# Optimization experiments

Measured on AMD Instinct MI355X. Metric: run time of the kernel, lower is better.

The kernel has to match this reference:

```python
import jax, jax.numpy as jnp
import numpy as np

B, C, H, W = 8, 256, 128, 128
SH, SW = 8, 8            # stoken_size
HH, WW = H // SH, W // SW
NH = 8                   # num_heads
HD = C // NH             # head_dim = 32
KD = HD                  # key_dim (attn_ratio=1)
ATTN_SCALE = KD ** (-0.5)
AFF_SCALE = C ** (-0.5)


def unfold9(x):
    """x: (B,C,hh,ww) -> (B, hh*ww, C, 9); matches Unfold(3) + transpose/reshape."""
    b, c, hh, ww = x.shape
    xp = jnp.pad(x, ((0, 0), (0, 0), (1, 1), (1, 1)))
    p = jnp.stack([xp[:, :, dy:dy + hh, dx:dx + ww]
                   for dy in range(3) for dx in range(3)], axis=2)  # (B,C,9,hh,ww)
    return p.transpose(0, 3, 4, 1, 2).reshape(b, hh * ww, c, 9)


def fold9(y):
    """y: (B,C,9,hh,ww) -> (B,C,hh,ww); matches Fold(3) (conv_transpose with identity kernels)."""
    hh, ww = y.shape[-2:]
    yp = jnp.pad(y, ((0, 0), (0, 0), (0, 0), (1, 1), (1, 1)))
    out = 0.
    for dy in range(3):
        for dx in range(3):
            out = out + yp[:, :, dy * 3 + dx, 2 - dy:2 - dy + hh, 2 - dx:2 - dx + ww]
    return out


def attention(sf, w_qkv, w_pe, w_proj):
    """Attention module with attn_ratio=1 (Conv layers have act=False, BN identity)."""
    b, c, hh, ww = sf.shape
    n = hh * ww
    qkv = jnp.einsum('oc,bchw->bohw', w_qkv, sf).reshape(b, NH, 2 * KD + HD, n)
    q, k, v = jnp.split(qkv, [KD, 2 * KD], axis=2)
    attn = jax.nn.softmax(jnp.einsum('bhkn,bhkm->bhnm', q, k) * ATTN_SCALE, axis=-1)
    o = jnp.einsum('bhdm,bhnm->bhdn', v, attn).reshape(b, c, hh, ww)
    pe = jax.lax.conv_general_dilated(
        v.reshape(b, c, hh, ww), w_pe, (1, 1), ((1, 1), (1, 1)),
        dimension_numbers=('NCHW', 'OIHW', 'NCHW'), feature_group_count=c)
    return jnp.einsum('oc,bchw->bohw', w_proj, o + pe)


def setup_inputs() -> dict:
    key = jax.random.key(0)
    k0, k1, k2, k3 = jax.random.split(key, 4)
    x = jax.random.normal(k0, (B, C, H, W), dtype=jnp.float32)
    w_qkv = jax.random.normal(k1, (3 * C, C), dtype=jnp.float32) * 0.05
    w_pe = jax.random.normal(k2, (C, 1, 3, 3), dtype=jnp.float32) * 0.05
    w_proj = jax.random.normal(k3, (C, C), dtype=jnp.float32) * 0.05
    return {'x': x, 'w_qkv': w_qkv, 'w_pe': w_pe, 'w_proj': w_proj}


def reference(x, w_qkv, w_pe, w_proj):
    # H,W divisible by stoken_size -> no padding branch
    xb = x.reshape(B, C, HH, SH, WW, SW)
    stoken = xb.mean(axis=(3, 5))                                   # (B,C,hh,ww) adaptive_avg_pool2d
    pix = xb.transpose(0, 2, 4, 3, 5, 1).reshape(B, HH * WW, SH * SW, C)
    # --- single no-grad iteration (n_iter=1) ---
    sf9 = unfold9(stoken)                                            # (B,n,C,9)
    aff = jax.nn.softmax(jnp.einsum('bnpc,bnck->bnpk', pix, sf9) * AFF_SCALE, axis=-1)
    aff = jax.lax.stop_gradient(aff)                                 # torch.no_grad
    asum = aff.sum(axis=2).transpose(0, 2, 1).reshape(B, 1, 9, HH, WW)
    asum = jax.lax.stop_gradient(fold9(asum))                        # (B,1,hh,ww)
    # --- super-token aggregation ---
    sf = jnp.einsum('bnpc,bnpk->bnck', pix, aff)                     # (B,n,C,9)
    sf = fold9(sf.transpose(0, 2, 3, 1).reshape(B, C, 9, HH, WW))    # (B,C,hh,ww)
    sf = sf / (asum + 1e-12)
    # --- refine with attention ---
    sf = attention(sf, w_qkv, w_pe, w_proj)
    # --- scatter back to pixels ---
    sf9b = unfold9(sf)                                               # (B,n,C,9)
    pix_out = jnp.einsum('bnck,bnpk->bnpc', sf9b, aff)               # (B,n,h*w,C)
    return pix_out.reshape(B, HH, WW, C, SH, SW).transpose(0, 3, 1, 4, 2, 5).reshape(B, C, H, W)
```

## Files before the change

### kernel.cpp

```cpp
#include <hip/hip_runtime.h>
#include <cstdint>
#include <cstddef>


#define AFF_SCALE 0.0625f
#define ATTN_SCALE 0.17677669529663687f

__global__ __launch_bounds__(128) void stoken_kernel(
    const float* __restrict__ x, float* __restrict__ stok_pad)
{
    int blk = blockIdx.x;
    int i  = blk & 15;
    int bc = blk >> 4;
    int t  = threadIdx.x;
    const float* xr = x + ((size_t)bc * 128 + i * 8) * 128 + t;
    float s = 0.f;
#pragma unroll
    for (int r = 0; r < 8; ++r) s += xr[r * 128];
    s += __shfl_down(s, 4, 64);
    s += __shfl_down(s, 2, 64);
    s += __shfl_down(s, 1, 64);
    if ((t & 7) == 0) {
        int j = t >> 3;
        int b = bc >> 8, c = bc & 255;
        stok_pad[(((size_t)b * 18 + (i + 1)) * 18 + (j + 1)) * 256 + c] =
            s * (1.f / 64.f);
    }
}

__global__ __launch_bounds__(256) void aff_agg_kernel(
    const float* __restrict__ x, const float* __restrict__ stok_pad,
    float* __restrict__ aff_g, float* __restrict__ asum_g,
    float* __restrict__ agg)
{
    __shared__ __align__(16) float pixs[256 * 68];
    __shared__ __align__(16) float sfs[9 * 260];
    __shared__ __align__(16) float part[576];

    int bid  = blockIdx.x;
    int xcd  = bid & 7, slot_ = bid >> 3;
    int pair = xcd * 128 + (slot_ >> 1);
    int m = pair & 7, i = (pair >> 3) & 15, b = pair >> 7;
    int j = m * 2 + (slot_ & 1);
    int bn = b * 256 + i * 16 + j;
    int t = threadIdx.x;

    {
        int c0 = t >> 3, pi = t & 7;
#pragma unroll
        for (int it = 0; it < 8; ++it) {
            int c = c0 + 32 * it;
            const float* xp = x + (((size_t)b * 256 + c) * 128 + i * 8 + pi) * 128 + j * 8;
            float4 f0 = *(const float4*)&xp[0];
            float4 f1 = *(const float4*)&xp[4];
            int gma = (c >> 2) & 3;
            int s0 = (2 * pi) ^ gma, s1 = (2 * pi + 1) ^ gma;
            *(float4*)&pixs[c * 68 + s0 * 4] = f0;
            *(float4*)&pixs[c * 68 + s1 * 4] = f1;
        }
    }
    {
        const float* spT = stok_pad + (size_t)b * 324 * 256;
#pragma unroll
        for (int dy = 0; dy < 3; ++dy)
#pragma unroll
            for (int dx = 0; dx < 3; ++dx)
                sfs[(dy * 3 + dx) * 260 + t] =
                    spT[((size_t)(i + dy) * 18 + (j + dx)) * 256 + t];
    }
    part[t] = 0.f;
    part[t + 256] = 0.f;
    if (t < 64) part[t + 512] = 0.f;
    __syncthreads();

    int w = t >> 6, l = t & 63;

    {
        int pq = l >> 2, cgl = l & 3;
        int cbase = w * 64 + cgl * 16;
        float acc[4][9];
#pragma unroll
        for (int ii = 0; ii < 4; ++ii)
#pragma unroll
            for (int k = 0; k < 9; ++k) acc[ii][k] = 0.f;

#pragma unroll
        for (int c4i = 0; c4i < 4; ++c4i) {
            int c = cbase + c4i * 4;
            int slot = (pq ^ c4i) * 4;
            const float4 p0 = *(const float4*)&pixs[(c + 0) * 68 + slot];
            const float4 p1 = *(const float4*)&pixs[(c + 1) * 68 + slot];
            const float4 p2 = *(const float4*)&pixs[(c + 2) * 68 + slot];
            const float4 p3 = *(const float4*)&pixs[(c + 3) * 68 + slot];
#pragma unroll
            for (int k = 0; k < 9; ++k) {
                const float4 sv = *(const float4*)&sfs[k * 260 + c];
                acc[0][k] += p0.x * sv.x + p1.x * sv.y + p2.x * sv.z + p3.x * sv.w;
                acc[1][k] += p0.y * sv.x + p1.y * sv.y + p2.y * sv.z + p3.y * sv.w;
                acc[2][k] += p0.z * sv.x + p1.z * sv.y + p2.z * sv.z + p3.z * sv.w;
                acc[3][k] += p0.w * sv.x + p1.w * sv.y + p2.w * sv.z + p3.w * sv.w;
            }
        }
#pragma unroll
        for (int ii = 0; ii < 4; ++ii)
#pragma unroll
            for (int k = 0; k < 9; ++k) {
                acc[ii][k] += __shfl_xor(acc[ii][k], 1, 64);
                acc[ii][k] += __shfl_xor(acc[ii][k], 2, 64);
            }
#pragma unroll
        for (int k = 0; k < 9; ++k) {
            float v01 = (cgl & 1) ? acc[1][k] : acc[0][k];
            float v23 = (cgl & 1) ? acc[3][k] : acc[2][k];
            float vk  = (cgl & 2) ? v23 : v01;
            atomicAdd(&part[l * 9 + k], vk);
        }
    }
    __syncthreads();

    float* affs = sfs;

    if (t < 64) {
        float a[9];
        float mx = -1e30f;
#pragma unroll
        for (int k = 0; k < 9; ++k) {
            float v = part[t * 9 + k] * AFF_SCALE;
            a[k] = v;
            mx = fmaxf(mx, v);
        }
        float ssum = 0.f;
#pragma unroll
        for (int k = 0; k < 9; ++k) { a[k] = __expf(a[k] - mx); ssum += a[k]; }
        float inv = 1.f / ssum;
#pragma unroll
        for (int k = 0; k < 9; ++k) {
            a[k] *= inv;
            affs[k * 64 + t] = a[k];
            aff_g[(size_t)bn * 576 + k * 64 + t] = a[k];
        }
#pragma unroll
        for (int k = 0; k < 9; ++k) {
            float r = a[k];
            r += __shfl_down(r, 32, 64); r += __shfl_down(r, 16, 64);
            r += __shfl_down(r, 8, 64);  r += __shfl_down(r, 4, 64);
            r += __shfl_down(r, 2, 64);  r += __shfl_down(r, 1, 64);
            if (t == 0) asum_g[(size_t)bn * 9 + k] = r;
        }
    }
    __syncthreads();

    {
        int cql = l >> 2, pq2 = l & 3;
        int cb2 = w * 64 + cql * 4;
        int gma = cql & 3;
        float acc2[4][9];
#pragma unroll
        for (int ii = 0; ii < 4; ++ii)
#pragma unroll
            for (int k = 0; k < 9; ++k) acc2[ii][k] = 0.f;

#pragma unroll
        for (int pp = 0; pp < 4; ++pp) {
            int p4 = pq2 * 4 + pp;
            int slot = (p4 ^ gma) * 4;
            const float4 q0 = *(const float4*)&pixs[(cb2 + 0) * 68 + slot];
            const float4 q1 = *(const float4*)&pixs[(cb2 + 1) * 68 + slot];
            const float4 q2 = *(const float4*)&pixs[(cb2 + 2) * 68 + slot];
            const float4 q3 = *(const float4*)&pixs[(cb2 + 3) * 68 + slot];
#pragma unroll
            for (int k = 0; k < 9; ++k) {
                const float4 av = *(const float4*)&affs[k * 64 + p4 * 4];
                acc2[0][k] += q0.x * av.x + q0.y * av.y + q0.z * av.z + q0.w * av.w;
                acc2[1][k] += q1.x * av.x + q1.y * av.y + q1.z * av.z + q1.w * av.w;
                acc2[2][k] += q2.x * av.x + q2.y * av.y + q2.z * av.z + q2.w * av.w;
                acc2[3][k] += q3.x * av.x + q3.y * av.y + q3.z * av.z + q3.w * av.w;
            }
        }
#pragma unroll
        for (int ii = 0; ii < 4; ++ii)
#pragma unroll
            for (int k = 0; k < 9; ++k) {
                acc2[ii][k] += __shfl_xor(acc2[ii][k], 1, 64);
                acc2[ii][k] += __shfl_xor(acc2[ii][k], 2, 64);
            }
        int cout = w * 64 + l;
#pragma unroll
        for (int k = 0; k < 9; ++k) {
            float v01 = (pq2 & 1) ? acc2[1][k] : acc2[0][k];
            float v23 = (pq2 & 1) ? acc2[3][k] : acc2[2][k];
            float vk  = (pq2 & 2) ? v23 : v01;
            agg[((size_t)bn * 9 + k) * 256 + cout] = vk;
        }
    }
}

__global__ __launch_bounds__(256) void fold_div_kernel(
    const float* __restrict__ agg, const float* __restrict__ asum_g,
    float* __restrict__ sf)
{
    __shared__ float v[256 * 17];
    int b = blockIdx.x >> 4, y = blockIdx.x & 15;
    int t = threadIdx.x;
    for (int x = 0; x < 16; ++x) {
        float af = 0.f, val = 0.f;
#pragma unroll
        for (int dy = 0; dy < 3; ++dy)
#pragma unroll
            for (int dx = 0; dx < 3; ++dx) {
                int ii = y + 1 - dy, jj = x + 1 - dx;
                if ((unsigned)ii < 16u && (unsigned)jj < 16u) {
                    int idx = (b * 256 + ii * 16 + jj) * 9 + dy * 3 + dx;
                    af  += asum_g[idx];
                    val += agg[(size_t)idx * 256 + t];
                }
            }
        v[t * 17 + x] = val / (af + 1e-12f);
    }
    __syncthreads();
    int xw = t & 15, cw0 = t >> 4;
#pragma unroll
    for (int it = 0; it < 16; ++it) {
        int c = cw0 + it * 16;
        sf[((size_t)b * 256 + c) * 256 + y * 16 + xw] = v[c * 17 + xw];
    }
}

__global__ __launch_bounds__(256) void gemm_w(
    const float* __restrict__ A, const float* __restrict__ Bm,
    float* __restrict__ Cout, int M, int mode)
{
    __shared__ float As[32 * 68];
    __shared__ float Bs[32 * 64];
    int b = blockIdx.x, o0 = blockIdx.y * 64, n0 = blockIdx.z * 64;
    int t = threadIdx.x;
    int tr = t >> 4, tc = t & 15;
    const float* Bb = Bm + (size_t)b * 256 * 256;
    float acc[4][4];
#pragma unroll
    for (int ii = 0; ii < 4; ++ii)
#pragma unroll
        for (int jj = 0; jj < 4; ++jj) acc[ii][jj] = 0.f;

    for (int k0 = 0; k0 < 256; k0 += 32) {
        {
            int ol = t >> 2, kq = (t & 3) * 8;
            const float* Ap = A + (size_t)(o0 + ol) * 256 + k0 + kq;
            const float4 f0 = *(const float4*)&Ap[0];
            const float4 f1 = *(const float4*)&Ap[4];
            As[(kq + 0) * 68 + ol] = f0.x; As[(kq + 1) * 68 + ol] = f0.y;
            As[(kq + 2) * 68 + ol] = f0.z; As[(kq + 3) * 68 + ol] = f0.w;
            As[(kq + 4) * 68 + ol] = f1.x; As[(kq + 5) * 68 + ol] = f1.y;
            As[(kq + 6) * 68 + ol] = f1.z; As[(kq + 7) * 68 + ol] = f1.w;
        }
#pragma unroll
        for (int i2 = 0; i2 < 8; ++i2) {
            int e = t + i2 * 256;
            int kl = e >> 6, nl = e & 63;
            Bs[kl * 64 + nl] = Bb[(size_t)(k0 + kl) * 256 + n0 + nl];
        }
        __syncthreads();
#pragma unroll
        for (int kk = 0; kk < 32; ++kk) {
            const float4 av = *(const float4*)&As[kk * 68 + tr * 4];
            const float4 bv = *(const float4*)&Bs[kk * 64 + tc * 4];
            acc[0][0] += av.x * bv.x; acc[0][1] += av.x * bv.y; acc[0][2] += av.x * bv.z; acc[0][3] += av.x * bv.w;
            acc[1][0] += av.y * bv.x; acc[1][1] += av.y * bv.y; acc[1][2] += av.y * bv.z; acc[1][3] += av.y * bv.w;
            acc[2][0] += av.z * bv.x; acc[2][1] += av.z * bv.y; acc[2][2] += av.z * bv.z; acc[2][3] += av.z * bv.w;
            acc[3][0] += av.w * bv.x; acc[3][1] += av.w * bv.y; acc[3][2] += av.w * bv.z; acc[3][3] += av.w * bv.w;
        }
        __syncthreads();
    }

    if (mode == 0) {
#pragma unroll
        for (int ii = 0; ii < 4; ++ii) {
            int o = o0 + tr * 4 + ii;
            float4 st = make_float4(acc[ii][0], acc[ii][1], acc[ii][2], acc[ii][3]);
            *(float4*)&Cout[((size_t)b * M + o) * 256 + n0 + tc * 4] = st;
        }
    } else {
#pragma unroll
        for (int jj = 0; jj < 4; ++jj) {
            int n = n0 + tc * 4 + jj;
            int y = n >> 4, x = n & 15;
            float4 st = make_float4(acc[0][jj], acc[1][jj], acc[2][jj], acc[3][jj]);
            *(float4*)&Cout[(((size_t)b * 18 + 1 + y) * 18 + 1 + x) * 256 + o0 + tr * 4] = st;
        }
    }
}

__global__ __launch_bounds__(256) void attn_kernel(
    const float* __restrict__ qkv, float* __restrict__ o_attn)
{
    __shared__ float smem[9216];
    int b = blockIdx.x, h = blockIdx.y, nt = blockIdx.z;
    int t = threadIdx.x, nl = t & 63, mq = t >> 6;
    int n = nt * 64 + nl;

    {
        int dd = t >> 3, mb = (t & 7) * 32;
        const float* krow = qkv + ((size_t)b * 768 + h * 96 + 32 + dd) * 256;
#pragma unroll
        for (int e4 = 0; e4 < 8; ++e4) {
            int m = mb + e4 * 4;
            const float4 kw = *(const float4*)&krow[m];
            smem[(m + 0) * 32 + dd] = kw.x; smem[(m + 1) * 32 + dd] = kw.y;
            smem[(m + 2) * 32 + dd] = kw.z; smem[(m + 3) * 32 + dd] = kw.w;
        }
    }
    float q[32];
    {
        const float* qbase = qkv + ((size_t)b * 768 + h * 96) * 256 + n;
#pragma unroll
        for (int d = 0; d < 32; ++d) q[d] = qbase[(size_t)d * 256];
    }
    __syncthreads();

    float l[64];
#pragma unroll
    for (int e = 0; e < 64; ++e) {
        const float* kp = &smem[(mq * 64 + e) * 32];
        float s = 0.f;
#pragma unroll
        for (int d4 = 0; d4 < 8; ++d4) {
            const float4 kv4 = *(const float4*)&kp[d4 * 4];
            s += q[d4 * 4 + 0] * kv4.x + q[d4 * 4 + 1] * kv4.y +
                 q[d4 * 4 + 2] * kv4.z + q[d4 * 4 + 3] * kv4.w;
        }
        l[e] = s * ATTN_SCALE;
    }
    float mx = -1e30f;
#pragma unroll
    for (int e = 0; e < 64; ++e) mx = fmaxf(mx, l[e]);
    float sm = 0.f;
#pragma unroll
    for (int e = 0; e < 64; ++e) { l[e] = __expf(l[e] - mx); sm += l[e]; }
    __syncthreads();

    {
        int dd = t >> 3, mb = (t & 7) * 32;
        const float* vrow = qkv + ((size_t)b * 768 + h * 96 + 64 + dd) * 256;
#pragma unroll
        for (int e4 = 0; e4 < 8; ++e4) {
            int m = mb + e4 * 4;
            const float4 vw = *(const float4*)&vrow[m];
            smem[(m + 0) * 32 + dd] = vw.x; smem[(m + 1) * 32 + dd] = vw.y;
            smem[(m + 2) * 32 + dd] = vw.z; smem[(m + 3) * 32 + dd] = vw.w;
        }
    }
    __syncthreads();

    float oa[32];
#pragma unroll
    for (int d = 0; d < 32; ++d) oa[d] = 0.f;
#pragma unroll
    for (int e = 0; e < 64; ++e) {
        float pm = l[e];
        const float* vp = &smem[(mq * 64 + e) * 32];
#pragma unroll
        for (int d4 = 0; d4 < 8; ++d4) {
            const float4 vv = *(const float4*)&vp[d4 * 4];
            oa[d4 * 4 + 0] += pm * vv.x; oa[d4 * 4 + 1] += pm * vv.y;
            oa[d4 * 4 + 2] += pm * vv.z; oa[d4 * 4 + 3] += pm * vv.w;
        }
    }
    __syncthreads();

    float* op   = smem;
    float* mxsm = smem + 8448;
    {
        int idx = mq * 64 + nl;
#pragma unroll
        for (int d = 0; d < 32; ++d) op[idx * 33 + d] = oa[d];
        mxsm[idx * 2 + 0] = mx;
        mxsm[idx * 2 + 1] = sm;
    }
    __syncthreads();

    if (t < 64) {
        float M2 = -1e30f;
#pragma unroll
        for (int q4 = 0; q4 < 4; ++q4) M2 = fmaxf(M2, mxsm[(q4 * 64 + t) * 2]);
        float w[4], S = 0.f;
#pragma unroll
        for (int q4 = 0; q4 < 4; ++q4) {
            w[q4] = __expf(mxsm[(q4 * 64 + t) * 2] - M2);
            S += mxsm[(q4 * 64 + t) * 2 + 1] * w[q4];
        }
        float inv = 1.f / S;
#pragma unroll
        for (int d = 0; d < 32; ++d) {
            float o = 0.f;
#pragma unroll
            for (int q4 = 0; q4 < 4; ++q4) o += op[(q4 * 64 + t) * 33 + d] * w[q4];
            o_attn[((size_t)b * 256 + h * 32 + d) * 256 + nt * 64 + t] = o * inv;
        }
    }
}

__global__ __launch_bounds__(256) void peadd_kernel(
    const float* __restrict__ qkv, const float* __restrict__ w_pe,
    float* __restrict__ o_attn)
{
    int bc = blockIdx.x;
    int b = bc >> 8, c = bc & 255;
    int t = threadIdx.x;
    int y = t >> 4, x = t & 15;
    int h = c >> 5, d = c & 31;
    const float* v = qkv + ((size_t)b * 768 + h * 96 + 64 + d) * 256;
    float acc = o_attn[(size_t)bc * 256 + t];
#pragma unroll
    for (int ky = 0; ky < 3; ++ky)
#pragma unroll
        for (int kx = 0; kx < 3; ++kx) {
            int yy = y + ky - 1, xx = x + kx - 1;
            if ((unsigned)yy < 16u && (unsigned)xx < 16u)
                acc += w_pe[c * 9 + ky * 3 + kx] * v[yy * 16 + xx];
        }
    o_attn[(size_t)bc * 256 + t] = acc;
}

__global__ __launch_bounds__(256) void scatter_kernel(
    const float* __restrict__ sfa_pad, const float* __restrict__ aff_g,
    float* __restrict__ out)
{
    __shared__ float ss[3 * 18 * 40];
    __shared__ float aff_s[16 * 577];

    int blk = blockIdx.x;
    int pi = blk & 7, i = (blk >> 3) & 15, b = blk >> 7;
    int t = threadIdx.x;

    for (int e = t; e < 1728; e += 256) {
        int dy = e / 576, rem = e % 576;
        int col = rem >> 5, idx = rem & 31;
        int q = idx >> 3, d = idx & 7;
        ss[(dy * 18 + col) * 40 + idx] =
            sfa_pad[(((size_t)b * 18 + i + dy) * 18 + col) * 256 + q * 64 + pi * 8 + d];
    }
    {
        const float* ag = aff_g + ((size_t)b * 256 + i * 16) * 576;
        for (int e = t; e < 9216; e += 256) {
            int j = e / 576, rem = e % 576;
            int k = rem >> 6, p = rem & 63;
            aff_s[j * 577 + p * 9 + k] = ag[j * 576 + rem];
        }
    }
    __syncthreads();

    int lane = t & 63, w = t >> 6;
    int j0 = lane >> 3, pj = lane & 7;
    int j1 = j0 + 8;

    float S0[4][9], S1[4][9];
#pragma unroll
    for (int q = 0; q < 4; ++q)
#pragma unroll
        for (int k = 0; k < 9; ++k) {
            int dy = k / 3, dx = k % 3;
            S0[q][k] = ss[(dy * 18 + j0 + dx) * 40 + q * 8 + pj];
            S1[q][k] = ss[(dy * 18 + j1 + dx) * 40 + q * 8 + pj];
        }

    int y = i * 8 + pi;
    size_t ob = (size_t)b * 256 * 16384 + (size_t)y * 128;
    const float* A0 = &aff_s[j0 * 577];
    const float* A1 = &aff_s[j1 * 577];
    for (int p = w * 16; p < w * 16 + 16; ++p) {
        float a0[9], a1[9];
#pragma unroll
        for (int k = 0; k < 9; ++k) { a0[k] = A0[p * 9 + k]; a1[k] = A1[p * 9 + k]; }
#pragma unroll
        for (int q = 0; q < 4; ++q) {
            int c2 = p * 4 + q;
            float v0 = 0.f, v1 = 0.f;
#pragma unroll
            for (int k = 0; k < 9; ++k) {
                v0 += S0[q][k] * a0[k];
                v1 += S1[q][k] * a1[k];
            }
            out[ob + (size_t)c2 * 16384 + lane] = v0;
            out[ob + (size_t)c2 * 16384 + 64 + lane] = v1;
        }
    }
}

extern "C" void kernel_launch(void* const* d_in, const int* in_sizes, int n_in,
                              void* d_out, int out_size, void* d_ws, size_t ws_size,
                              hipStream_t stream) {
    const float* x      = (const float*)d_in[0];
    const float* w_qkv  = (const float*)d_in[1];
    const float* w_pe   = (const float*)d_in[2];
    const float* w_proj = (const float*)d_in[3];
    float* out = (float*)d_out;
    float* agg = (float*)d_out;

    float* ws = (float*)d_ws;
    const size_t o_aff  = 0;
    const size_t o_asum = 1179648;
    const size_t o_pad  = 1198080;
    const size_t o_sf   = 1861632;
    const size_t o_qkv  = 2385920;

    hipMemsetAsync(ws + o_pad, 0, 663552 * sizeof(float), stream);

    stoken_kernel<<<8 * 256 * 16, 128, 0, stream>>>(x, ws + o_pad);
    aff_agg_kernel<<<8 * 256, 256, 0, stream>>>(x, ws + o_pad, ws + o_aff,
                                                ws + o_asum, agg);
    fold_div_kernel<<<8 * 16, 256, 0, stream>>>(agg, ws + o_asum, ws + o_sf);
    gemm_w<<<dim3(8, 12, 4), 256, 0, stream>>>(w_qkv, ws + o_sf, ws + o_qkv, 768, 0);
    hipMemsetAsync(ws + o_pad, 0, 663552 * sizeof(float), stream);
    attn_kernel<<<dim3(8, 8, 4), 256, 0, stream>>>(ws + o_qkv, ws + o_sf);
    peadd_kernel<<<8 * 256, 256, 0, stream>>>(ws + o_qkv, w_pe, ws + o_sf);
    gemm_w<<<dim3(8, 4, 4), 256, 0, stream>>>(w_proj, ws + o_sf, ws + o_pad, 256, 1);
    scatter_kernel<<<8 * 16 * 8, 256, 0, stream>>>(ws + o_pad, ws + o_aff, out);
}
```

Before: 442.9 us.

## Fuse PE conv into attention, drop pad memsets, DPP reductions, smaller proj tiles

Removes both hipMemsetAsync calls on the padded buffer by predicating border reads in the consumer kernels. The depthwise positional-encoding conv is folded into attn_kernel, reading V from shared memory, which removes a separate kernel launch and an extra read/write pass over o_attn. Cross-lane reductions switch from shfl_xor to DPP quad permutes. The projection GEMM gets its own kernel with 32-row output tiles, doubling block count for more parallelism. Attention shared memory grows because it no longer aliases op and kv, which may lower occupancy.

```diff
diff --git a/kernel.cpp b/kernel.cpp
--- a/kernel.cpp
+++ b/kernel.cpp
@@ -5,6 +5,15 @@
 
 #define AFF_SCALE 0.0625f
 #define ATTN_SCALE 0.17677669529663687f
+
+__device__ __forceinline__ float dpp_add_xor1(float v) {
+    int p = __builtin_amdgcn_update_dpp(0, __float_as_int(v), 0xB1, 0xF, 0xF, true);
+    return v + __int_as_float(p);
+}
+__device__ __forceinline__ float dpp_add_xor2(float v) {
+    int p = __builtin_amdgcn_update_dpp(0, __float_as_int(v), 0x4E, 0xF, 0xF, true);
+    return v + __int_as_float(p);
+}
 
 __global__ __launch_bounds__(128) void stoken_kernel(
     const float* __restrict__ x, float* __restrict__ stok_pad)
@@ -64,9 +73,13 @@
 #pragma unroll
         for (int dy = 0; dy < 3; ++dy)
 #pragma unroll
-            for (int dx = 0; dx < 3; ++dx)
-                sfs[(dy * 3 + dx) * 260 + t] =
-                    spT[((size_t)(i + dy) * 18 + (j + dx)) * 256 + t];
+            for (int dx = 0; dx < 3; ++dx) {
+                int r = i + dy, cn = j + dx;
+                float v = 0.f;
+                if ((unsigned)(r - 1) < 16u && (unsigned)(cn - 1) < 16u)
+                    v = spT[((size_t)r * 18 + cn) * 256 + t];
+                sfs[(dy * 3 + dx) * 260 + t] = v;
+            }
     }
     part[t] = 0.f;
     part[t + 256] = 0.f;
@@ -105,8 +118,8 @@
         for (int ii = 0; ii < 4; ++ii)
 #pragma unroll
             for (int k = 0; k < 9; ++k) {
-                acc[ii][k] += __shfl_xor(acc[ii][k], 1, 64);
-                acc[ii][k] += __shfl_xor(acc[ii][k], 2, 64);
+                acc[ii][k] = dpp_add_xor1(acc[ii][k]);
+                acc[ii][k] = dpp_add_xor2(acc[ii][k]);
             }
 #pragma unroll
         for (int k = 0; k < 9; ++k) {
@@ -181,8 +194,8 @@
         for (int ii = 0; ii < 4; ++ii)
 #pragma unroll
             for (int k = 0; k < 9; ++k) {
-                acc2[ii][k] += __shfl_xor(acc2[ii][k], 1, 64);
-                acc2[ii][k] += __shfl_xor(acc2[ii][k], 2, 64);
+                acc2[ii][k] = dpp_add_xor1(acc2[ii][k]);
+                acc2[ii][k] = dpp_add_xor2(acc2[ii][k]);
             }
         int cout = w * 64 + l;
 #pragma unroll
@@ -228,7 +241,7 @@
 
 __global__ __launch_bounds__(256) void gemm_w(
     const float* __restrict__ A, const float* __restrict__ Bm,
-    float* __restrict__ Cout, int M, int mode)
+    float* __restrict__ Cout, int M)
 {
     __shared__ float As[32 * 68];
     __shared__ float Bs[32 * 64];
@@ -272,28 +285,74 @@
         __syncthreads();
     }
 
-    if (mode == 0) {
-#pragma unroll
-        for (int ii = 0; ii < 4; ++ii) {
-            int o = o0 + tr * 4 + ii;
-            float4 st = make_float4(acc[ii][0], acc[ii][1], acc[ii][2], acc[ii][3]);
-            *(float4*)&Cout[((size_t)b * M + o) * 256 + n0 + tc * 4] = st;
-        }
-    } else {
-#pragma unroll
-        for (int jj = 0; jj < 4; ++jj) {
-            int n = n0 + tc * 4 + jj;
-            int y = n >> 4, x = n & 15;
-            float4 st = make_float4(acc[0][jj], acc[1][jj], acc[2][jj], acc[3][jj]);
-            *(float4*)&Cout[(((size_t)b * 18 + 1 + y) * 18 + 1 + x) * 256 + o0 + tr * 4] = st;
-        }
+#pragma unroll
+    for (int ii = 0; ii < 4; ++ii) {
+        int o = o0 + tr * 4 + ii;
+        float4 st = make_float4(acc[ii][0], acc[ii][1], acc[ii][2], acc[ii][3]);
+        *(float4*)&Cout[((size_t)b * M + o) * 256 + n0 + tc * 4] = st;
+    }
+}
+
+__global__ __launch_bounds__(256) void gemm_proj32(
+    const float* __restrict__ A, const float* __restrict__ Bm,
+    float* __restrict__ Cout)
+{
+    __shared__ float As[32 * 36];
+    __shared__ float Bs[32 * 64];
+    int b = blockIdx.x, o0 = blockIdx.y * 32, n0 = blockIdx.z * 64;
+    int t = threadIdx.x;
+    int tr = t >> 4, tc = t & 15;
+    const float* Bb = Bm + (size_t)b * 256 * 256;
+    float acc[2][4];
+#pragma unroll
+    for (int ii = 0; ii < 2; ++ii)
+#pragma unroll
+        for (int jj = 0; jj < 4; ++jj) acc[ii][jj] = 0.f;
+
+    for (int k0 = 0; k0 < 256; k0 += 32) {
+        {
+            int ol = t & 31, kq = (t >> 5) * 4;
+            const float* Ap = A + (size_t)(o0 + ol) * 256 + k0 + kq;
+            const float4 f = *(const float4*)&Ap[0];
+            As[(kq + 0) * 36 + ol] = f.x; As[(kq + 1) * 36 + ol] = f.y;
+            As[(kq + 2) * 36 + ol] = f.z; As[(kq + 3) * 36 + ol] = f.w;
+        }
+#pragma unroll
+        for (int i2 = 0; i2 < 8; ++i2) {
+            int e = t + i2 * 256;
+            int kl = e >> 6, nl = e & 63;
+            Bs[kl * 64 + nl] = Bb[(size_t)(k0 + kl) * 256 + n0 + nl];
+        }
+        __syncthreads();
+#pragma unroll
+        for (int kk = 0; kk < 32; ++kk) {
+            const float2 av = *(const float2*)&As[kk * 36 + tr * 2];
+            const float4 bv = *(const float4*)&Bs[kk * 64 + tc * 4];
+            acc[0][0] += av.x * bv.x; acc[0][1] += av.x * bv.y;
+            acc[0][2] += av.x * bv.z; acc[0][3] += av.x * bv.w;
+            acc[1][0] += av.y * bv.x; acc[1][1] += av.y * bv.y;
+            acc[1][2] += av.y * bv.z; acc[1][3] += av.y * bv.w;
+        }
+        __syncthreads();
+    }
+
+#pragma unroll
+    for (int jj = 0; jj < 4; ++jj) {
+        int n = n0 + tc * 4 + jj;
+        int y = n >> 4, x = n & 15;
+        float2 st = make_float2(acc[0][jj], acc[1][jj]);
+        *(float2*)&Cout[(((size_t)b * 18 + 1 + y) * 18 + 1 + x) * 256 + o0 + tr * 2] = st;
     }
 }
 
 __global__ __launch_bounds__(256) void attn_kernel(
-    const float* __restrict__ qkv, float* __restrict__ o_attn)
-{
-    __shared__ float smem[9216];
+    const float* __restrict__ qkv, const float* __restrict__ w_pe,
+    float* __restrict__ o_attn)
+{
+    __shared__ float kv[8192];
+    __shared__ float op[256 * 33];
+    __shared__ float mxsm[512];
+    __shared__ float wpe_s[288];
     int b = blockIdx.x, h = blockIdx.y, nt = blockIdx.z;
     int t = threadIdx.x, nl = t & 63, mq = t >> 6;
     int n = nt * 64 + nl;
@@ -305,10 +364,12 @@
         for (int e4 = 0; e4 < 8; ++e4) {
             int m = mb + e4 * 4;
             const float4 kw = *(const float4*)&krow[m];
-            smem[(m + 0) * 32 + dd] = kw.x; smem[(m + 1) * 32 + dd] = kw.y;
-            smem[(m + 2) * 32 + dd] = kw.z; smem[(m + 3) * 32 + dd] = kw.w;
-        }
-    }
+            kv[(m + 0) * 32 + dd] = kw.x; kv[(m + 1) * 32 + dd] = kw.y;
+            kv[(m + 2) * 32 + dd] = kw.z; kv[(m + 3) * 32 + dd] = kw.w;
+        }
+    }
+    for (int e = t; e < 288; e += 256) wpe_s[e] = w_pe[h * 288 + e];
+
     float q[32];
     {
         const float* qbase = qkv + ((size_t)b * 768 + h * 96) * 256 + n;
@@ -320,7 +381,7 @@
     float l[64];
 #pragma unroll
     for (int e = 0; e < 64; ++e) {
-        const float* kp = &smem[(mq * 64 + e) * 32];
+        const float* kp = &kv[(mq * 64 + e) * 32];
         float s = 0.f;
 #pragma unroll
         for (int d4 = 0; d4 < 8; ++d4) {
@@ -345,8 +406,8 @@
         for (int e4 = 0; e4 < 8; ++e4) {
             int m = mb + e4 * 4;
             const float4 vw = *(const float4*)&vrow[m];
-            smem[(m + 0) * 32 + dd] = vw.x; smem[(m + 1) * 32 + dd] = vw.y;
-            smem[(m + 2) * 32 + dd] = vw.z; smem[(m + 3) * 32 + dd] = vw.w;
+            kv[(m + 0) * 32 + dd] = vw.x; kv[(m + 1) * 32 + dd] = vw.y;
+            kv[(m + 2) * 32 + dd] = vw.z; kv[(m + 3) * 32 + dd] = vw.w;
         }
     }
     __syncthreads();
@@ -357,7 +418,7 @@
 #pragma unroll
     for (int e = 0; e < 64; ++e) {
         float pm = l[e];
-        const float* vp = &smem[(mq * 64 + e) * 32];
+        const float* vp = &kv[(mq * 64 + e) * 32];
 #pragma unroll
         for (int d4 = 0; d4 < 8; ++d4) {
             const float4 vv = *(const float4*)&vp[d4 * 4];
@@ -365,10 +426,7 @@
             oa[d4 * 4 + 2] += pm * vv.z; oa[d4 * 4 + 3] += pm * vv.w;
         }
     }
-    __syncthreads();
-
-    float* op   = smem;
-    float* mxsm = smem + 8448;
+
     {
         int idx = mq * 64 + nl;
 #pragma unroll
@@ -389,36 +447,25 @@
             S += mxsm[(q4 * 64 + t) * 2 + 1] * w[q4];
         }
         float inv = 1.f / S;
+        int n2 = nt * 64 + t;
+        int yy0 = n2 >> 4, xx0 = n2 & 15;
 #pragma unroll
         for (int d = 0; d < 32; ++d) {
             float o = 0.f;
 #pragma unroll
             for (int q4 = 0; q4 < 4; ++q4) o += op[(q4 * 64 + t) * 33 + d] * w[q4];
-            o_attn[((size_t)b * 256 + h * 32 + d) * 256 + nt * 64 + t] = o * inv;
-        }
-    }
-}
-
-__global__ __launch_bounds__(256) void peadd_kernel(
-    const float* __restrict__ qkv, const float* __restrict__ w_pe,
-    float* __restrict__ o_attn)
-{
-    int bc = blockIdx.x;
-    int b = bc >> 8, c = bc & 255;
-    int t = threadIdx.x;
-    int y = t >> 4, x = t & 15;
-    int h = c >> 5, d = c & 31;
-    const float* v = qkv + ((size_t)b * 768 + h * 96 + 64 + d) * 256;
-    float acc = o_attn[(size_t)bc * 256 + t];
-#pragma unroll
-    for (int ky = 0; ky < 3; ++ky)
-#pragma unroll
-        for (int kx = 0; kx < 3; ++kx) {
-            int yy = y + ky - 1, xx = x + kx - 1;
-            if ((unsigned)yy < 16u && (unsigned)xx < 16u)
-                acc += w_pe[c * 9 + ky * 3 + kx] * v[yy * 16 + xx];
-        }
-    o_attn[(size_t)bc * 256 + t] = acc;
+            float pe = 0.f;
+#pragma unroll
+            for (int ky = 0; ky < 3; ++ky)
+#pragma unroll
+                for (int kx = 0; kx < 3; ++kx) {
+                    int yv = yy0 + ky - 1, xv = xx0 + kx - 1;
+                    if ((unsigned)yv < 16u && (unsigned)xv < 16u)
+                        pe += wpe_s[d * 9 + ky * 3 + kx] * kv[(yv * 16 + xv) * 32 + d];
+                }
+            o_attn[((size_t)b * 256 + h * 32 + d) * 256 + n2] = o * inv + pe;
+        }
+    }
 }
 
 __global__ __launch_bounds__(256) void scatter_kernel(
@@ -436,8 +483,11 @@
         int dy = e / 576, rem = e % 576;
         int col = rem >> 5, idx = rem & 31;
         int q = idx >> 3, d = idx & 7;
-        ss[(dy * 18 + col) * 40 + idx] =
-            sfa_pad[(((size_t)b * 18 + i + dy) * 18 + col) * 256 + q * 64 + pi * 8 + d];
+        int row = i + dy;
+        float v = 0.f;
+        if ((unsigned)(row - 1) < 16u && (unsigned)(col - 1) < 16u)
+            v = sfa_pad[(((size_t)b * 18 + row) * 18 + col) * 256 + q * 64 + pi * 8 + d];
+        ss[(dy * 18 + col) * 40 + idx] = v;
     }
     {
         const float* ag = aff_g + ((size_t)b * 256 + i * 16) * 576;
@@ -503,16 +553,12 @@
     const size_t o_sf   = 1861632;
     const size_t o_qkv  = 2385920;
 
-    hipMemsetAsync(ws + o_pad, 0, 663552 * sizeof(float), stream);
-
     stoken_kernel<<<8 * 256 * 16, 128, 0, stream>>>(x, ws + o_pad);
     aff_agg_kernel<<<8 * 256, 256, 0, stream>>>(x, ws + o_pad, ws + o_aff,
                                                 ws + o_asum, agg);
     fold_div_kernel<<<8 * 16, 256, 0, stream>>>(agg, ws + o_asum, ws + o_sf);
-    gemm_w<<<dim3(8, 12, 4), 256, 0, stream>>>(w_qkv, ws + o_sf, ws + o_qkv, 768, 0);
-    hipMemsetAsync(ws + o_pad, 0, 663552 * sizeof(float), stream);
-    attn_kernel<<<dim3(8, 8, 4), 256, 0, stream>>>(ws + o_qkv, ws + o_sf);
-    peadd_kernel<<<8 * 256, 256, 0, stream>>>(ws + o_qkv, w_pe, ws + o_sf);
-    gemm_w<<<dim3(8, 4, 4), 256, 0, stream>>>(w_proj, ws + o_sf, ws + o_pad, 256, 1);
+    gemm_w<<<dim3(8, 12, 4), 256, 0, stream>>>(w_qkv, ws + o_sf, ws + o_qkv, 768);
+    attn_kernel<<<dim3(8, 8, 4), 256, 0, stream>>>(ws + o_qkv, w_pe, ws + o_sf);
+    gemm_proj32<<<dim3(8, 8, 4), 256, 0, stream>>>(w_proj, ws + o_sf, ws + o_pad);
     scatter_kernel<<<8 * 16 * 8, 256, 0, stream>>>(ws + o_pad, ws + o_aff, out);
 }
```

After: 459.3 us. 1.04x slower.
